# Kernel tuning notes

Hardware: AMD Instinct MI355X
Metric: run time of the kernel (lower is better)

The kernel has to match this reference:

```python
import jax, jax.numpy as jnp
import numpy as np

B, C, H, W = 16, 256, 64, 64
NH, DH = 8, 64
POS_C = 4


def setup_inputs() -> dict:
    key = jax.random.key(0)
    ks = jax.random.split(key, 10)
    cin = C + POS_C
    dqkv = NH * DH
    sc = 1.0 / np.sqrt(cin)
    inp = {
        "x": jax.random.normal(ks[0], (B, C, H, W), dtype=jnp.float32),
        "pos_emb": jax.random.normal(ks[1], (1, POS_C, H, W), dtype=jnp.float32) / np.sqrt(C * H * W),
        "Wk": jax.random.normal(ks[2], (dqkv, cin), dtype=jnp.float32) * sc,
        "bk": jnp.zeros((dqkv,), dtype=jnp.float32),
        "Wq": jax.random.normal(ks[3], (dqkv, cin), dtype=jnp.float32) * sc,
        "bq": jnp.zeros((dqkv,), dtype=jnp.float32),
        "Wv": jax.random.normal(ks[4], (dqkv, cin), dtype=jnp.float32) * sc,
        "bv": jnp.zeros((dqkv,), dtype=jnp.float32),
        "Wo": jax.random.normal(ks[5], (C, dqkv), dtype=jnp.float32) / np.sqrt(dqkv),
        "bo": jnp.zeros((C,), dtype=jnp.float32),
    }
    return inp


def _conv1x1(w, b, x):
    # w: (out, in), x: (B, in, H, W) -> (B, out, H, W)
    return jnp.einsum('oc,bchw->bohw', w, x) + b[None, :, None, None]


def reference(x, pos_emb, Wk, bk, Wq, bq, Wv, bv, Wo, bo):
    b, c, h, w = x.shape
    xp = jnp.concatenate([x, jnp.broadcast_to(pos_emb, (b, POS_C, h, w))], axis=1)
    K = _conv1x1(Wk, bk, xp).reshape(b, NH, DH, h, w)
    Q = _conv1x1(Wq, bq, xp).reshape(b, NH, DH, h, w)
    V = _conv1x1(Wv, bv, xp).reshape(b, NH, DH, h, w)
    # Row (width-axis) logits: (B, nh, H, W, W)
    qk_w = jnp.einsum('bhdij,bhdik->bhijk', Q, K)
    # Column (height-axis) logits: (B, nh, H, W, H)
    qk_h = jnp.einsum('bhdij,bhdkj->bhijk', Q, K)
    scale = 1.0 / np.sqrt(w + h)
    p = jax.nn.softmax(jnp.concatenate([qk_w, qk_h], axis=-1) * scale, axis=-1)
    p_w, p_h = p[..., :w], p[..., w:]
    a_w = jnp.einsum('bhijk,bhdik->bhdij', p_w, V)
    a_h = jnp.einsum('bhijk,bhdkj->bhdij', p_h, V)
    A = (a_w + a_h).reshape(b, NH * DH, h, w)
    return x + _conv1x1(Wo, bo, A)
```

## Files before the change

### kernel.cpp

```cpp
#include <hip/hip_runtime.h>

typedef unsigned short u16;
typedef __bf16 bf16x8 __attribute__((ext_vector_type(8)));
typedef float f32x4 __attribute__((ext_vector_type(4)));
typedef unsigned short u16x8 __attribute__((ext_vector_type(8)));
typedef unsigned short u16x4 __attribute__((ext_vector_type(4)));

#define MFMA16(A,B,C) __builtin_amdgcn_mfma_f32_16x16x32_bf16(A,B,C,0,0,0)

__device__ __forceinline__ float b2f(u16 h){ unsigned u = ((unsigned)h)<<16; return __builtin_bit_cast(float,u); }
__device__ __forceinline__ u16 f2b(float f){ unsigned u = __builtin_bit_cast(unsigned,f); u += 0x7fffu + ((u>>16)&1u); return (u16)(u>>16); }
__device__ __forceinline__ bf16x8 ldb8(const u16* p){ return __builtin_bit_cast(bf16x8, *(const u16x8*)p); }

__device__ __forceinline__ void g2lds16(const u16* g, u16* l){
  __builtin_amdgcn_global_load_lds((const __attribute__((address_space(1))) void*)g,
                                   (__attribute__((address_space(3))) void*)l, 16, 0, 0);
}


__global__ void k_prep_w(const float* __restrict__ Wq, const float* __restrict__ Wk,
                         const float* __restrict__ Wv, const float* __restrict__ bq,
                         const float* __restrict__ bk, const float* __restrict__ bv,
                         const float* __restrict__ Wo,
                         u16* __restrict__ WP, u16* __restrict__ BIAS,
                         u16* __restrict__ WoP){
  int r = blockIdx.x;
  int tid = threadIdx.x;
  if (r < 1536){
    int t = r >> 9, rm = r & 511;
    const float* src = (t==0 ? Wq : (t==1 ? Wk : Wv)) + (long)rm*260;
    WP[(long)r*288 + tid] = f2b(src[tid]);
    if (tid < 32) WP[(long)r*288 + 256 + tid] = (tid < 4) ? f2b(src[256 + tid]) : (u16)0;
    if (tid == 0){
      const float* bs = (t==0 ? bq : (t==1 ? bk : bv));
      BIAS[r] = f2b(bs[rm]);
    }
  } else {
    int co = r - 1536;
    WoP[(long)co*512 + tid]       = f2b(Wo[(long)co*512 + tid]);
    WoP[(long)co*512 + 256 + tid] = f2b(Wo[(long)co*512 + 256 + tid]);
  }
}

__global__ void k_sentinel(float* __restrict__ out){
  long i = (long)blockIdx.x*256 + threadIdx.x;
  out[i] = 100.0f;
}

__global__ __launch_bounds__(256) void k_cvtx(const float* __restrict__ x,
                                              const float* __restrict__ pos,
                                              u16* __restrict__ XT, int b0){
  __shared__ u16 tile[64*65];
  int bidx = blockIdx.x;
  int ct = bidx & 3, pt = (bidx>>2)&63, bl = bidx>>8;
  int c0 = ct*64, p0 = pt*64;
  int tid = threadIdx.x;
  const float* xb = x + (long)(b0+bl)*256*4096;
  #pragma unroll
  for (int it=0; it<16; ++it){
    int idx = it*256 + tid; int cc = idx>>6, px = idx&63;
    tile[cc*65 + px] = f2b(xb[(long)(c0+cc)*4096 + p0 + px]);
  }
  __syncthreads();
  u16* dst = XT + ((long)(bl*4096 + p0))*288 + c0;
  #pragma unroll
  for (int it=0; it<4; ++it){
    int idx = it*256 + tid; int pp = idx>>4, c4 = (idx&15)*4;
    u16x4 o;
    #pragma unroll
    for (int u=0;u<4;++u) o[u] = tile[(c4+u)*65 + pp];
    *(u16x4*)&dst[(long)pp*288 + c4] = o;
  }
  if (ct == 0){
    int px = tid>>2, c8 = (tid&3)*8;
    u16x8 o;
    #pragma unroll
    for (int u=0;u<8;++u){
      int c = c8 + u;
      o[u] = (c < 4) ? f2b(pos[(long)c*4096 + p0 + px]) : (u16)0;
    }
    *(u16x8*)&XT[((long)(bl*4096 + p0 + px))*288 + 256 + c8] = o;
  }
}

__global__ __launch_bounds__(256) void k_qkv(
    const u16* __restrict__ XT, const u16* __restrict__ WP,
    const u16* __restrict__ BIAS,
    u16* __restrict__ Qb, u16* __restrict__ Kb, u16* __restrict__ Vt, int nwg){
  __shared__ u16 sW[2][128*32];
  __shared__ u16 sX[2][128*32];
  int hw = blockIdx.x;
  int bidx = (hw & 7)*(nwg >> 3) + (hw >> 3);
  int mt = bidx % 12; long nt = bidx / 12;
  int oc0 = mt*128; long p0 = nt*128;
  int bl = (int)(p0>>12); int pl0 = (int)(p0 & 4095);
  int tid = threadIdx.x;
  int wid = tid>>6, lane = tid&63, l16 = lane&15, qd = lane>>4;
  int wm = wid>>1, wn = wid&1;
  int srow = lane>>2, sc8 = (lane&3)*8;
  f32x4 zf = {0.f,0.f,0.f,0.f};
  f32x4 acc[4][4];
  #pragma unroll
  for (int i=0;i<4;++i){
    #pragma unroll
    for (int j=0;j<4;++j) acc[i][j] = zf;
  }
  auto stage = [&](int buf, int kk){
    #pragma unroll
    for (int c=0;c<2;++c){
      int seg = wid*2 + c;
      int row = seg*16 + srow;
      g2lds16(&WP[(long)(oc0+row)*288 + kk + sc8], &sW[buf][seg*512]);
      g2lds16(&XT[(p0 + row)*288 + kk + sc8],      &sX[buf][seg*512]);
    }
  };
  stage(0, 0);
  #pragma unroll
  for (int t=0; t<9; ++t){
    __syncthreads();
    if (t < 8) stage((t+1)&1, (t+1)*32);
    int cur = t&1;
    bf16x8 a[4], bb[4];
    #pragma unroll
    for (int mi=0;mi<4;++mi) a[mi]  = ldb8(&sW[cur][(wm*64+mi*16+l16)*32 + qd*8]);
    #pragma unroll
    for (int ni=0;ni<4;++ni) bb[ni] = ldb8(&sX[cur][(wn*64+ni*16+l16)*32 + qd*8]);
    #pragma unroll
    for (int mi=0;mi<4;++mi){
      #pragma unroll
      for (int ni=0;ni<4;++ni)
        acc[mi][ni] = MFMA16(a[mi], bb[ni], acc[mi][ni]);
    }
  }
  #pragma unroll
  for (int mi=0;mi<4;++mi){
    int mbase = wm*64 + mi*16 + qd*4;
    int ocb = oc0 + mbase;
    int t = ocb>>9, ocm = ocb&511;
    int hh = ocm>>6, dd = ocm&63;
    float bv4[4];
    #pragma unroll
    for (int r=0;r<4;++r) bv4[r] = b2f(BIAS[ocb + r]);
    #pragma unroll
    for (int ni=0;ni<4;++ni){
      int n = wn*64 + ni*16 + l16;
      int pl = pl0 + n;
      if (t < 2){
        u16* dstb = (t==0? Qb : Kb);
        u16x4 pk;
        #pragma unroll
        for (int r=0;r<4;++r) pk[r] = f2b(acc[mi][ni][r] + bv4[r]);
        *(u16x4*)&dstb[((long)(bl*8+hh)*4096 + pl)*64 + dd] = pk;
      } else {
        long base = (long)(bl*8+hh)*262144 + (long)dd*4096 + pl;
        #pragma unroll
        for (int r=0;r<4;++r) Vt[base + (long)r*4096] = f2b(acc[mi][ni][r] + bv4[r]);
      }
    }
  }
}

__global__ __launch_bounds__(256) void k_vtr(const u16* __restrict__ Vt,
                                             u16* __restrict__ Vtc){
  __shared__ u16 tile[64*68];
  int bid = blockIdx.x;
  int d = bid & 63; long ph = bid >> 6;
  const u16* src = Vt + ph*262144 + (long)d*4096;
  u16* dst = Vtc + ph*262144 + (long)d*4096;
  int tid = threadIdx.x;
  #pragma unroll
  for (int it=0; it<2; ++it){
    int idx = it*256 + tid; int i = idx>>3, j8 = (idx&7)*8;
    u16x8 v = *(const u16x8*)&src[i*64 + j8];
    u16x4 lo = {v[0],v[1],v[2],v[3]}, hi = {v[4],v[5],v[6],v[7]};
    *(u16x4*)&tile[i*68 + j8]     = lo;
    *(u16x4*)&tile[i*68 + j8 + 4] = hi;
  }
  __syncthreads();
  #pragma unroll
  for (int it=0; it<2; ++it){
    int idx = it*256 + tid; int j = idx>>3, i8 = (idx&7)*8;
    u16x8 o;
    #pragma unroll
    for (int u=0;u<8;++u) o[u] = tile[(i8+u)*68 + j];
    *(u16x8*)&dst[j*64 + i8] = o;
  }
}

template<int COL>
__global__ __launch_bounds__(256) void k_attn(
    const u16* __restrict__ Qb, const u16* __restrict__ Kb,
    const u16* __restrict__ Vsrc, u16* __restrict__ U,
    float* __restrict__ M, float* __restrict__ L, int nwg){
  __shared__ u16 sm[4*64*72];
  u16* Qs = sm;
  u16* Ks = sm + 4608;
  u16* VT = sm + 9216;
  u16* Ps = sm + 13824;
  int hw = blockIdx.x;
  int bid = (hw & 7)*(nwg >> 3) + (hw >> 3);
  int rc = bid&63, h=(bid>>6)&7, bl=bid>>9;
  long plane  = (long)(bl*8+h)*262144;
  long sbase  = (long)(bl*8+h)*4096;
  int tid = threadIdx.x;
  #pragma unroll
  for (int it=0; it<2; ++it){
    int idx = it*256 + tid; int row = idx>>3, c8 = (idx&7)*8;
    long gqk = plane + ((long)(COL ? (row*64 + rc) : (rc*64 + row)))*64 + c8;
    *(u16x8*)&Qs[row*72 + c8] = *(const u16x8*)&Qb[gqk];
    *(u16x8*)&Ks[row*72 + c8] = *(const u16x8*)&Kb[gqk];
    long gv = plane + (long)row*4096 + rc*64 + c8;
    *(u16x8*)&VT[row*72 + c8] = *(const u16x8*)&Vsrc[gv];
  }
  __syncthreads();
  int wid = tid>>6, lane = tid&63, l16 = lane&15, qd = lane>>4;
  int j0 = wid*16;
  f32x4 zf = {0.f,0.f,0.f,0.f};
  f32x4 sv[4] = {zf,zf,zf,zf};
  #pragma unroll
  for (int d0=0; d0<64; d0+=32){
    bf16x8 a = ldb8(&Qs[(j0+l16)*72 + d0 + qd*8]);
    #pragma unroll
    for (int n=0;n<4;++n){
      bf16x8 bb = ldb8(&Ks[(n*16+l16)*72 + d0 + qd*8]);
      sv[n] = MFMA16(a, bb, sv[n]);
    }
  }
  const float scale = 0.08838834764831845f;
  float mrow[4], lrow[4];
  #pragma unroll
  for (int r=0;r<4;++r){
    float mv = -1e30f;
    #pragma unroll
    for (int n=0;n<4;++n){ sv[n][r] *= scale; mv = fmaxf(mv, sv[n][r]); }
    mv = fmaxf(mv, __shfl_xor(mv,1)); mv = fmaxf(mv, __shfl_xor(mv,2));
    mv = fmaxf(mv, __shfl_xor(mv,4)); mv = fmaxf(mv, __shfl_xor(mv,8));
    float ls = 0.f;
    #pragma unroll
    for (int n=0;n<4;++n){ float p = expf(fminf(sv[n][r]-mv, 0.f)); sv[n][r] = p; ls += p; }
    ls += __shfl_xor(ls,1); ls += __shfl_xor(ls,2);
    ls += __shfl_xor(ls,4); ls += __shfl_xor(ls,8);
    mrow[r]=mv; lrow[r]=ls;
    int qi = j0 + qd*4 + r;
    #pragma unroll
    for (int n=0;n<4;++n) Ps[qi*72 + n*16 + l16] = f2b(sv[n][r]);
  }
  __syncthreads();
  f32x4 u4[4] = {zf,zf,zf,zf};
  #pragma unroll
  for (int k0=0;k0<64;k0+=32){
    bf16x8 a = ldb8(&Ps[(j0+l16)*72 + k0 + qd*8]);
    #pragma unroll
    for (int n=0;n<4;++n){
      bf16x8 bb = ldb8(&VT[(n*16+l16)*72 + k0 + qd*8]);
      u4[n] = MFMA16(a, bb, u4[n]);
    }
  }
  if (!COL){
    #pragma unroll
    for (int r=0;r<4;++r){
      int qi = j0 + qd*4 + r;
      long pl = (long)rc*64 + qi;
      long ob = (sbase + pl)*64;
      #pragma unroll
      for (int n=0;n<4;++n) U[ob + n*16 + l16] = f2b(u4[n][r]);
      if (l16==0){ M[sbase+pl]=mrow[r]; L[sbase+pl]=lrow[r]; }
    }
  } else {
    #pragma unroll
    for (int r=0;r<4;++r){
      int qi = j0 + qd*4 + r;
      long pix = sbase + (long)qi*64 + rc;
      float mw = M[pix], lw = L[pix];
      float mh = mrow[r], lh = lrow[r];
      float m  = fmaxf(mw, mh);
      float ew = expf(fminf(mw - m, 0.f));
      float eh = expf(fminf(mh - m, 0.f));
      float rden = 1.f / fmaxf(ew*lw + eh*lh, 1e-20f);
      long ob = pix*64;
      #pragma unroll
      for (int n=0;n<4;++n){
        float uw = b2f(U[ob + n*16 + l16]);
        U[ob + n*16 + l16] = f2b((ew*uw + eh*u4[n][r])*rden);
      }
    }
  }
}

__global__ __launch_bounds__(256) void k_oproj(
    const u16* __restrict__ WoP, const float* __restrict__ bo,
    const u16* __restrict__ AC, const float* __restrict__ x,
    float* __restrict__ out, int b0, int nwg){
  __shared__ u16 sW[2][128*32];
  __shared__ u16 sA[2][128*32];
  int hw = blockIdx.x;
  int bidx = (hw & 7)*(nwg >> 3) + (hw >> 3);
  int mt = bidx & 1; long nt = bidx >> 1;
  int co0 = mt*128; long p0 = nt*128;
  int bl = (int)(p0>>12), pl0 = (int)(p0&4095);
  int gb = b0 + bl;
  int tid = threadIdx.x;
  int wid=tid>>6, lane=tid&63, l16=lane&15, qd=lane>>4;
  int wm=wid>>1, wn=wid&1;
  int srow = lane>>2, sc8 = (lane&3)*8;
  f32x4 zf = {0.f,0.f,0.f,0.f};
  f32x4 acc[4][4];
  #pragma unroll
  for (int i=0;i<4;++i){
    #pragma unroll
    for (int j=0;j<4;++j) acc[i][j] = zf;
  }
  auto stage = [&](int buf, int kk){
    #pragma unroll
    for (int c=0;c<2;++c){
      int seg = wid*2 + c;
      int row = seg*16 + srow;
      g2lds16(&WoP[(long)(co0+row)*512 + kk + sc8], &sW[buf][seg*512]);
      g2lds16(&AC[((long)(bl*8+(kk>>6))*4096 + pl0 + row)*64 + (kk&63) + sc8], &sA[buf][seg*512]);
    }
  };
  stage(0, 0);
  #pragma unroll
  for (int t=0; t<16; ++t){
    __syncthreads();
    if (t < 15) stage((t+1)&1, (t+1)*32);
    int cur = t&1;
    bf16x8 a[4], bb[4];
    #pragma unroll
    for (int mi=0;mi<4;++mi) a[mi]  = ldb8(&sW[cur][(wm*64+mi*16+l16)*32 + qd*8]);
    #pragma unroll
    for (int ni=0;ni<4;++ni) bb[ni] = ldb8(&sA[cur][(wn*64+ni*16+l16)*32 + qd*8]);
    #pragma unroll
    for (int mi=0;mi<4;++mi){
      #pragma unroll
      for (int ni=0;ni<4;++ni)
        acc[mi][ni] = MFMA16(a[mi], bb[ni], acc[mi][ni]);
    }
  }
  #pragma unroll
  for (int mi=0;mi<4;++mi){
    #pragma unroll
    for (int ni=0;ni<4;++ni){
      int n = wn*64+ni*16+l16; int pl = pl0+n;
      #pragma unroll
      for (int r=0;r<4;++r){
        int co = co0 + wm*64+mi*16+qd*4+r;
        long addr = ((long)(gb*256+co))*4096 + pl;
        out[addr] = acc[mi][ni][r] + bo[co] + x[addr];
      }
    }
  }
}

extern "C" void kernel_launch(void* const* d_in, const int* in_sizes, int n_in,
                              void* d_out, int out_size, void* d_ws, size_t ws_size,
                              hipStream_t stream) {
  (void)in_sizes; (void)n_in; (void)out_size;
  const float* x    = (const float*)d_in[0];
  const float* pos  = (const float*)d_in[1];
  const float* Wk   = (const float*)d_in[2];
  const float* bk   = (const float*)d_in[3];
  const float* Wq   = (const float*)d_in[4];
  const float* bq   = (const float*)d_in[5];
  const float* Wv   = (const float*)d_in[6];
  const float* bv   = (const float*)d_in[7];
  const float* Wo   = (const float*)d_in[8];
  const float* bo   = (const float*)d_in[9];
  float* out = (float*)d_out;
  char* ws = (char*)d_ws;

  const long per_batch = 23592960l;
  const long fixed = 1149952l;
  if (fixed + per_batch > (long)ws_size){
    k_sentinel<<<65536, 256, 0, stream>>>(out);
    return;
  }
  int CB = 16;
  while (CB > 1 && fixed + (long)CB*per_batch > (long)ws_size) CB >>= 1;

  u16*  WP   = (u16*)(ws);
  u16*  BIAS = (u16*)(ws + 884736l);
  u16*  WoP  = (u16*)(ws + 887808l);
  long base  = fixed;
  u16*  XT   = (u16*)(ws + base);
  u16*  Qc   = (u16*)(ws + base + (long)CB*2359296l);
  u16*  Kc   = (u16*)((char*)Qc  + (long)CB*4194304l);
  u16*  Vt   = (u16*)((char*)Kc  + (long)CB*4194304l);
  u16*  Vtc  = (u16*)((char*)Vt  + (long)CB*4194304l);
  u16*  Uw   = (u16*)((char*)Vtc + (long)CB*4194304l);
  float* MWc = (float*)((char*)Uw + (long)CB*4194304l);
  float* LWc = (float*)((char*)MWc + (long)CB*131072l);

  k_prep_w<<<1792, 256, 0, stream>>>(Wq, Wk, Wv, bq, bk, bv, Wo, WP, BIAS, WoP);
  for (int b0 = 0; b0 < 16; b0 += CB){
    k_cvtx    <<<CB*256, 256, 0, stream>>>(x, pos, XT, b0);
    k_qkv     <<<CB*384, 256, 0, stream>>>(XT, WP, BIAS, Qc, Kc, Vt, CB*384);
    k_vtr     <<<CB*512, 256, 0, stream>>>(Vt, Vtc);
    k_attn<0> <<<CB*512, 256, 0, stream>>>(Qc, Kc, Vt,  Uw, MWc, LWc, CB*512);
    k_attn<1> <<<CB*512, 256, 0, stream>>>(Qc, Kc, Vtc, Uw, MWc, LWc, CB*512);
    k_oproj   <<<CB*64,  256, 0, stream>>>(WoP, bo, Uw, x, out, b0, CB*64);
  }
}
```

Before: 442.2 us.

## Enlarge QKV GEMM tiles to 256x256 with a 512-thread pipelined K loop

```diff
diff --git a/kernel.cpp b/kernel.cpp
--- a/kernel.cpp
+++ b/kernel.cpp
@@ -16,6 +16,10 @@
   __builtin_amdgcn_global_load_lds((const __attribute__((address_space(1))) void*)g,
                                    (__attribute__((address_space(3))) void*)l, 16, 0, 0);
 }
+
+#define BAR   __builtin_amdgcn_s_barrier()
+#define LGKM0 do{ asm volatile("s_waitcnt lgkmcnt(0)" ::: "memory"); __builtin_amdgcn_sched_barrier(0); }while(0)
+#define VMC4  asm volatile("s_waitcnt vmcnt(4)" ::: "memory")
 
 
 __global__ void k_prep_w(const float* __restrict__ Wq, const float* __restrict__ Wk,
@@ -29,8 +33,8 @@
   if (r < 1536){
     int t = r >> 9, rm = r & 511;
     const float* src = (t==0 ? Wq : (t==1 ? Wk : Wv)) + (long)rm*260;
-    WP[(long)r*288 + tid] = f2b(src[tid]);
-    if (tid < 32) WP[(long)r*288 + 256 + tid] = (tid < 4) ? f2b(src[256 + tid]) : (u16)0;
+    WP[(long)r*320 + tid] = f2b(src[tid]);
+    if (tid < 64) WP[(long)r*320 + 256 + tid] = (tid < 4) ? f2b(src[256 + tid]) : (u16)0;
     if (tid == 0){
       const float* bs = (t==0 ? bq : (t==1 ? bk : bv));
       BIAS[r] = f2b(bs[rm]);
@@ -62,100 +66,160 @@
     tile[cc*65 + px] = f2b(xb[(long)(c0+cc)*4096 + p0 + px]);
   }
   __syncthreads();
-  u16* dst = XT + ((long)(bl*4096 + p0))*288 + c0;
+  u16* dst = XT + ((long)(bl*4096 + p0))*320 + c0;
   #pragma unroll
   for (int it=0; it<4; ++it){
     int idx = it*256 + tid; int pp = idx>>4, c4 = (idx&15)*4;
     u16x4 o;
     #pragma unroll
     for (int u=0;u<4;++u) o[u] = tile[(c4+u)*65 + pp];
-    *(u16x4*)&dst[(long)pp*288 + c4] = o;
+    *(u16x4*)&dst[(long)pp*320 + c4] = o;
   }
   if (ct == 0){
-    int px = tid>>2, c8 = (tid&3)*8;
-    u16x8 o;
-    #pragma unroll
-    for (int u=0;u<8;++u){
-      int c = c8 + u;
-      o[u] = (c < 4) ? f2b(pos[(long)c*4096 + p0 + px]) : (u16)0;
-    }
-    *(u16x8*)&XT[((long)(bl*4096 + p0 + px))*288 + 256 + c8] = o;
-  }
-}
-
-__global__ __launch_bounds__(256) void k_qkv(
+    int px = tid>>2, cb = (tid&3)*16;
+    u16* row = XT + ((long)(bl*4096 + p0 + px))*320 + 256 + cb;
+    #pragma unroll
+    for (int half=0; half<2; ++half){
+      u16x8 o;
+      #pragma unroll
+      for (int u=0;u<8;++u){
+        int c = cb + half*8 + u;
+        o[u] = (c < 4) ? f2b(pos[(long)c*4096 + p0 + px]) : (u16)0;
+      }
+      *(u16x8*)&row[half*8] = o;
+    }
+  }
+}
+
+__global__ __launch_bounds__(512,2) void k_qkv(
     const u16* __restrict__ XT, const u16* __restrict__ WP,
     const u16* __restrict__ BIAS,
     u16* __restrict__ Qb, u16* __restrict__ Kb, u16* __restrict__ Vt, int nwg){
-  __shared__ u16 sW[2][128*32];
-  __shared__ u16 sX[2][128*32];
+  __shared__ u16 sm[65536];
   int hw = blockIdx.x;
   int bidx = (hw & 7)*(nwg >> 3) + (hw >> 3);
-  int mt = bidx % 12; long nt = bidx / 12;
-  int oc0 = mt*128; long p0 = nt*128;
-  int bl = (int)(p0>>12); int pl0 = (int)(p0 & 4095);
+  int mt = bidx % 6; long nt = bidx / 6;
+  int oc0 = mt*256;
+  int bl = (int)(nt >> 4); int pl0 = ((int)nt & 15)*256;
   int tid = threadIdx.x;
   int wid = tid>>6, lane = tid&63, l16 = lane&15, qd = lane>>4;
-  int wm = wid>>1, wn = wid&1;
-  int srow = lane>>2, sc8 = (lane&3)*8;
+  int wm = wid>>2, wn = wid&3;
+  const u16* gA = WP + (long)oc0*320;
+  const u16* gB = XT + ((long)nt*256)*320;
+
   f32x4 zf = {0.f,0.f,0.f,0.f};
-  f32x4 acc[4][4];
-  #pragma unroll
-  for (int i=0;i<4;++i){
+  f32x4 acc[8][4];
+  #pragma unroll
+  for (int i=0;i<8;++i){
     #pragma unroll
     for (int j=0;j<4;++j) acc[i][j] = zf;
   }
-  auto stage = [&](int buf, int kk){
-    #pragma unroll
-    for (int c=0;c<2;++c){
-      int seg = wid*2 + c;
-      int row = seg*16 + srow;
-      g2lds16(&WP[(long)(oc0+row)*288 + kk + sc8], &sW[buf][seg*512]);
-      g2lds16(&XT[(p0 + row)*288 + kk + sc8],      &sX[buf][seg*512]);
-    }
+
+  auto stage2 = [&](const u16* g, int ldsOff){
+    g2lds16(g + (long)(wid*16 + (lane>>2))*320 + (lane&3)*8,       &sm[ldsOff + wid*512]);
+    g2lds16(g + (long)(128 + wid*16 + (lane>>2))*320 + (lane&3)*8, &sm[ldsOff + 4096 + wid*512]);
   };
-  stage(0, 0);
-  #pragma unroll
-  for (int t=0; t<9; ++t){
-    __syncthreads();
-    if (t < 8) stage((t+1)&1, (t+1)*32);
-    int cur = t&1;
-    bf16x8 a[4], bb[4];
-    #pragma unroll
-    for (int mi=0;mi<4;++mi) a[mi]  = ldb8(&sW[cur][(wm*64+mi*16+l16)*32 + qd*8]);
-    #pragma unroll
-    for (int ni=0;ni<4;++ni) bb[ni] = ldb8(&sX[cur][(wn*64+ni*16+l16)*32 + qd*8]);
-    #pragma unroll
-    for (int mi=0;mi<4;++mi){
-      #pragma unroll
-      for (int ni=0;ni<4;++ni)
-        acc[mi][ni] = MFMA16(a[mi], bb[ni], acc[mi][ni]);
-    }
-  }
-  #pragma unroll
-  for (int mi=0;mi<4;++mi){
-    int mbase = wm*64 + mi*16 + qd*4;
-    int ocb = oc0 + mbase;
-    int t = ocb>>9, ocm = ocb&511;
-    int hh = ocm>>6, dd = ocm&63;
-    float bv4[4];
-    #pragma unroll
-    for (int r=0;r<4;++r) bv4[r] = b2f(BIAS[ocb + r]);
-    #pragma unroll
-    for (int ni=0;ni<4;++ni){
-      int n = wn*64 + ni*16 + l16;
-      int pl = pl0 + n;
-      if (t < 2){
-        u16* dstb = (t==0? Qb : Kb);
+  auto aOff = [&](int buf,int ks){ return (buf*2+ks)*8192; };
+  auto bOff = [&](int buf,int ks){ return 32768 + (buf*2+ks)*8192; };
+
+  bf16x8 rA[4], rB[4];
+  auto ldA4 = [&](int buf,int ks,int mh){
+    int base = aOff(buf,ks) + (wm*128 + mh*64 + l16)*32 + qd*8;
+    #pragma unroll
+    for (int i=0;i<4;++i) rA[i] = ldb8(&sm[base + i*16*32]);
+  };
+  auto ldB4 = [&](int buf,int ks){
+    int base = bOff(buf,ks) + (wn*64 + l16)*32 + qd*8;
+    #pragma unroll
+    for (int i=0;i<4;++i) rB[i] = ldb8(&sm[base + i*16*32]);
+  };
+  auto mmac = [&](int mh){
+    __builtin_amdgcn_s_setprio(1);
+    #pragma unroll
+    for (int i=0;i<4;++i){
+      #pragma unroll
+      for (int j=0;j<4;++j)
+        acc[mh*4+i][j] = MFMA16(rA[i], rB[j], acc[mh*4+i][j]);
+    }
+    __builtin_amdgcn_s_setprio(0);
+  };
+
+  stage2(gA + 0,  aOff(0,0));
+  stage2(gB + 0,  bOff(0,0));
+  stage2(gA + 32, aOff(0,1));
+  stage2(gB + 32, bOff(0,1));
+  VMC4; BAR;
+
+  for (int t=0; t<5; ++t){
+    int cur = t&1, nxt = cur^1;
+    bool st = (t < 4);
+    int k1 = (t+1)*64;
+    ldB4(cur,0); ldA4(cur,0,0);
+    if (st) stage2(gA + k1, aOff(nxt,0));
+    BAR; LGKM0; mmac(0); BAR;
+    ldA4(cur,0,1);
+    if (st) stage2(gB + k1, bOff(nxt,0));
+    BAR; LGKM0; mmac(1); VMC4; BAR;
+    ldB4(cur,1); ldA4(cur,1,0);
+    if (st) stage2(gA + k1 + 32, aOff(nxt,1));
+    BAR; LGKM0; mmac(0); BAR;
+    ldA4(cur,1,1);
+    if (st) stage2(gB + k1 + 32, bOff(nxt,1));
+    BAR; LGKM0; mmac(1); VMC4; BAR;
+  }
+
+  if (oc0 < 1024){
+    const u16* dstb = (oc0 < 512) ? Qb : Kb;
+    #pragma unroll
+    for (int mi=0;mi<8;++mi){
+      int oc = oc0 + wm*128 + mi*16 + qd*4;
+      int ocm = oc & 511;
+      int hh = ocm>>6, dd = ocm&63;
+      float bv4[4];
+      #pragma unroll
+      for (int r=0;r<4;++r) bv4[r] = b2f(BIAS[oc + r]);
+      #pragma unroll
+      for (int ni=0;ni<4;++ni){
+        int pl = pl0 + wn*64 + ni*16 + l16;
         u16x4 pk;
         #pragma unroll
         for (int r=0;r<4;++r) pk[r] = f2b(acc[mi][ni][r] + bv4[r]);
-        *(u16x4*)&dstb[((long)(bl*8+hh)*4096 + pl)*64 + dd] = pk;
-      } else {
-        long base = (long)(bl*8+hh)*262144 + (long)dd*4096 + pl;
+        *(u16x4*)&((u16*)dstb)[((long)(bl*8+hh)*4096 + pl)*64 + dd] = pk;
+      }
+    }
+  } else {
+    #pragma unroll
+    for (int p=0;p<2;++p){
+      if (wm == p){
         #pragma unroll
-        for (int r=0;r<4;++r) Vt[base + (long)r*4096] = f2b(acc[mi][ni][r] + bv4[r]);
-      }
+        for (int mi=0;mi<8;++mi){
+          int ocl = mi*16 + qd*4;
+          float bv4[4];
+          #pragma unroll
+          for (int r=0;r<4;++r) bv4[r] = b2f(BIAS[oc0 + p*128 + ocl + r]);
+          #pragma unroll
+          for (int ni=0;ni<4;++ni){
+            int px = wn*64 + ni*16 + l16;
+            u16x4 pk;
+            #pragma unroll
+            for (int r=0;r<4;++r) pk[r] = f2b(acc[mi][ni][r] + bv4[r]);
+            *(u16x4*)&sm[px*136 + ocl] = pk;
+          }
+        }
+      }
+      BAR;
+      #pragma unroll
+      for (int it=0; it<8; ++it){
+        int c = it*512 + tid;
+        int ocr = c>>5, px8 = (c&31)*8;
+        u16x8 o;
+        #pragma unroll
+        for (int u=0;u<8;++u) o[u] = sm[(px8+u)*136 + ocr];
+        int ocm = (oc0 & 511) + p*128 + ocr;
+        int hh = ocm>>6, dd = ocm&63;
+        *(u16x8*)&Vt[(long)(bl*8+hh)*262144 + (long)dd*4096 + pl0 + px8] = o;
+      }
+      BAR;
     }
   }
 }
@@ -191,14 +255,13 @@
 __global__ __launch_bounds__(256) void k_attn(
     const u16* __restrict__ Qb, const u16* __restrict__ Kb,
     const u16* __restrict__ Vsrc, u16* __restrict__ U,
-    float* __restrict__ M, float* __restrict__ L, int nwg){
+    float* __restrict__ M, float* __restrict__ L){
   __shared__ u16 sm[4*64*72];
   u16* Qs = sm;
   u16* Ks = sm + 4608;
   u16* VT = sm + 9216;
   u16* Ps = sm + 13824;
-  int hw = blockIdx.x;
-  int bid = (hw & 7)*(nwg >> 3) + (hw >> 3);
+  int bid = blockIdx.x;
   int rc = bid&63, h=(bid>>6)&7, bl=bid>>9;
   long plane  = (long)(bl*8+h)*262144;
   long sbase  = (long)(bl*8+h)*4096;
@@ -369,8 +432,8 @@
   float* out = (float*)d_out;
   char* ws = (char*)d_ws;
 
-  const long per_batch = 23592960l;
-  const long fixed = 1149952l;
+  const long per_batch = 23855104l;
+  const long fixed = 1248256l;
   if (fixed + per_batch > (long)ws_size){
     k_sentinel<<<65536, 256, 0, stream>>>(out);
     return;
@@ -379,11 +442,11 @@
   while (CB > 1 && fixed + (long)CB*per_batch > (long)ws_size) CB >>= 1;
 
   u16*  WP   = (u16*)(ws);
-  u16*  BIAS = (u16*)(ws + 884736l);
-  u16*  WoP  = (u16*)(ws + 887808l);
+  u16*  BIAS = (u16*)(ws + 983040l);
+  u16*  WoP  = (u16*)(ws + 986112l);
   long base  = fixed;
   u16*  XT   = (u16*)(ws + base);
-  u16*  Qc   = (u16*)(ws + base + (long)CB*2359296l);
+  u16*  Qc   = (u16*)(ws + base + (long)CB*2621440l);
   u16*  Kc   = (u16*)((char*)Qc  + (long)CB*4194304l);
   u16*  Vt   = (u16*)((char*)Kc  + (long)CB*4194304l);
   u16*  Vtc  = (u16*)((char*)Vt  + (long)CB*4194304l);
@@ -394,10 +457,10 @@
   k_prep_w<<<1792, 256, 0, stream>>>(Wq, Wk, Wv, bq, bk, bv, Wo, WP, BIAS, WoP);
   for (int b0 = 0; b0 < 16; b0 += CB){
     k_cvtx    <<<CB*256, 256, 0, stream>>>(x, pos, XT, b0);
-    k_qkv     <<<CB*384, 256, 0, stream>>>(XT, WP, BIAS, Qc, Kc, Vt, CB*384);
+    k_qkv     <<<CB*96,  512, 0, stream>>>(XT, WP, BIAS, Qc, Kc, Vt, CB*96);
     k_vtr     <<<CB*512, 256, 0, stream>>>(Vt, Vtc);
-    k_attn<0> <<<CB*512, 256, 0, stream>>>(Qc, Kc, Vt,  Uw, MWc, LWc, CB*512);
-    k_attn<1> <<<CB*512, 256, 0, stream>>>(Qc, Kc, Vtc, Uw, MWc, LWc, CB*512);
+    k_attn<0> <<<CB*512, 256, 0, stream>>>(Qc, Kc, Vt,  Uw, MWc, LWc);
+    k_attn<1> <<<CB*512, 256, 0, stream>>>(Qc, Kc, Vtc, Uw, MWc, LWc);
     k_oproj   <<<CB*64,  256, 0, stream>>>(WoP, bo, Uw, x, out, b0, CB*64);
   }
 }
```

New measurement: 516.8 us. +16.9%, slower.
